# Optimization experiments

Hardware: AMD Instinct MI355X
Metric: run time of the kernel (lower is better)

Reference implementation:

```python
import jax, jax.numpy as jnp
import numpy as np

B, T, E, H = 256, 200, 512, 8
NEG = -(2.0 ** 32) + 1.0  # padding value used by the TF implementation


def _pos_table(T, E):
    # sin/cos positional encoding exactly as in PositionEncoding.build
    pos = np.arange(T)[:, None].astype(np.float64)
    i = np.arange(E)[None, :]
    angle = pos / np.power(10000.0, 2.0 * (i // 2) / E)
    pe = np.where(i % 2 == 0, np.sin(angle), np.cos(angle))
    return jnp.asarray(pe, dtype=jnp.float32)


def setup_inputs() -> dict:
    key = jax.random.key(0)
    ks = jax.random.split(key, 9)
    tn = lambda k, shape, std: (jax.random.truncated_normal(k, -2.0, 2.0, shape, jnp.float32) * std)
    glorot = lambda k, shape: jax.random.uniform(k, shape, jnp.float32,
                                                 -np.sqrt(6.0 / (shape[0] + shape[1])),
                                                 np.sqrt(6.0 / (shape[0] + shape[1])))
    return {
        "queries": jax.random.normal(ks[0], (B, T, E), jnp.float32),
        "keys": jax.random.normal(ks[1], (B, T, E), jnp.float32),
        "query_len": jax.random.randint(ks[2], (B, 1), 1, T + 1),
        "key_len": jax.random.randint(ks[3], (B, 1), 1, T + 1),
        "pos_q": _pos_table(T, E),
        "pos_k": _pos_table(T, E),
        "W_Q": tn(ks[4], (E, E), 0.05),
        "W_K": tn(ks[5], (E, E), 0.05),
        "W_V": tn(ks[6], (E, E), 0.05),
        "fw1": glorot(ks[7], (E, 4 * E)),
        "fw2": glorot(ks[8], (4 * E, E)),
    }


def reference(queries, keys, query_len, key_len, pos_q, pos_k, W_Q, W_K, W_V, fw1, fw2):
    Bq, Tq, Eq = queries.shape
    Dh = Eq // H
    dt = queries.dtype
    neg = jnp.asarray(NEG, dt)

    # positional encoding: scaled table added to inputs
    scale = jnp.asarray(Eq, dt) ** 0.5
    q_in = queries + pos_q * scale          # (B,T,E)
    k_in = keys + pos_k * scale

    # sequence masks from lengths (B,1) -> (B,T)
    ar = jnp.arange(Tq)[None, :]
    q_mask = (ar < query_len).astype(dt)
    k_mask = (ar < key_len).astype(dt)

    # projections, split into heads
    Q = (q_in @ W_Q).reshape(Bq, Tq, H, Dh)
    K_ = (k_in @ W_K).reshape(Bq, Tq, H, Dh)
    V = (k_in @ W_V).reshape(Bq, Tq, H, Dh)

    # scaled dot-product attention  (B,H,Tq,Tk)
    scores = jnp.einsum('bqhd,bkhd->bhqk', Q, K_) / jnp.asarray(Dh, dt) ** 0.5
    scores = jnp.where(k_mask[:, None, None, :] > 0, scores, neg)
    # blinding: mask the diagonal (query attends to itself)
    eye = jnp.eye(Tq, dtype=bool)
    scores = jnp.where(eye[None, None], neg, scores)
    scores = scores - jnp.max(scores, axis=-1, keepdims=True)
    attn = jax.nn.softmax(scores, axis=-1)
    attn = attn * q_mask[:, None, :, None]

    out = jnp.einsum('bhqk,bkhd->bqhd', attn, V).reshape(Bq, Tq, Eq)

    # residual (use_res=True), no layer norm (use_layer_norm=False)
    out = out + q_in

    # pointwise feed-forward + residual
    ff = jax.nn.relu(out @ fw1) @ fw2
    out = out + ff

    # output_type == 'mean'
    return jnp.mean(out, axis=1, keepdims=True)  # (B,1,E)
```

## Files before the change

### kernel.cpp

```cpp
#include <hip/hip_runtime.h>

#define B_   256
#define T_   200
#define E_   512
#define H_   8
#define Dh_  64
#define F_   2048
#define M_   (B_ * T_)
#define MH_  (M_ / 2)
#define SCALE 22.62741699796952f
#define NEGV  -4294967296.0f

typedef __attribute__((ext_vector_type(8))) short bf16x8;
typedef __attribute__((ext_vector_type(4))) float f32x4;

__device__ __forceinline__ float bf2f(unsigned short u) {
    union { unsigned u32; float f; } v; v.u32 = ((unsigned)u) << 16; return v.f;
}
__device__ __forceinline__ unsigned short f2bf(float f) {
    union { float f32; unsigned u; } v; v.f32 = f;
    unsigned r = v.u + 0x7FFFu + ((v.u >> 16) & 1u);
    return (unsigned short)(r >> 16);
}
__device__ __forceinline__ unsigned pack_hilo(float f) {
    unsigned short hi = f2bf(f);
    unsigned short lo = f2bf(f - bf2f(hi));
    return (unsigned)hi | ((unsigned)lo << 16);
}
__device__ __forceinline__ void load_lds16(const unsigned short* g, unsigned short* l) {
    __builtin_amdgcn_global_load_lds(
        (const __attribute__((address_space(1))) unsigned int*)g,
        (__attribute__((address_space(3))) unsigned int*)l, 16, 0, 0);
}

__global__ __launch_bounds__(256) void k_prep(
    float* __restrict__ q, float* __restrict__ k,
    const float* __restrict__ pos_q, const float* __restrict__ pos_k)
{
    const int z = blockIdx.y;
    float* X = z ? k : q;
    const float* Ps = z ? pos_k : pos_q;
    size_t idx = ((size_t)blockIdx.x * 256 + threadIdx.x) * 4;
    int row = (int)(idx >> 9);
    int col = (int)(idx & 511);
    int t = row % T_;
    float4 v = *(const float4*)&X[idx];
    float4 p = *(const float4*)&Ps[(size_t)t * E_ + col];
    uint4 o;
    o.x = pack_hilo(v.x + p.x * SCALE);
    o.y = pack_hilo(v.y + p.y * SCALE);
    o.z = pack_hilo(v.z + p.z * SCALE);
    o.w = pack_hilo(v.w + p.w * SCALE);
    *(uint4*)&X[idx] = o;
}

__global__ __launch_bounds__(256) void k_trw(
    const float* __restrict__ in, unsigned short* __restrict__ oh,
    unsigned short* __restrict__ ol)
{
    const int k0 = blockIdx.x * 64, n0 = blockIdx.y * 64;
    const int tid = threadIdx.x;
    __shared__ unsigned short th[64][65], tl[64][65];
#pragma unroll
    for (int i = 0; i < 16; i++) {
        int e = i * 256 + tid;
        int r = e >> 6, c = e & 63;
        float f = in[(size_t)(k0 + r) * 512 + n0 + c];
        unsigned short h = f2bf(f);
        th[r][c] = h;
        tl[r][c] = f2bf(f - bf2f(h));
    }
    __syncthreads();
#pragma unroll
    for (int i = 0; i < 16; i++) {
        int e = i * 256 + tid;
        int r = e >> 6, c = e & 63;
        oh[(size_t)(n0 + r) * 512 + k0 + c] = th[c][r];
        ol[(size_t)(n0 + r) * 512 + k0 + c] = tl[c][r];
    }
}

template<int NPROD, bool SPLIT>
__global__ __launch_bounds__(256) void k_projx(
    const unsigned int* __restrict__ Apk,
    const unsigned short* __restrict__ Bh,
    const unsigned short* __restrict__ Bl,
    unsigned short* __restrict__ Chi,
    unsigned short* __restrict__ Clo)
{
    const int K = 512, N = 512;
    __shared__ alignas(16) unsigned short AsH[128 * 32];
    __shared__ alignas(16) unsigned short AsL[128 * 32];
    __shared__ alignas(16) unsigned short BsH[128 * 32];
    __shared__ alignas(16) unsigned short BsL[(NPROD >= 3) ? 128 * 32 : 8];

    const int tid = threadIdx.x;
    const int w = tid >> 6, lane = tid & 63;
    const int m0 = blockIdx.x * 128, n0 = blockIdx.y * 128;
    const int mr = lane & 15, q = lane >> 4;

    f32x4 acc[4][4];
#pragma unroll
    for (int i = 0; i < 4; i++)
#pragma unroll
        for (int j = 0; j < 4; j++) acc[i][j] = (f32x4){0.f, 0.f, 0.f, 0.f};

    const int c0  = w * 64 + lane;
    const int c1  = 256 + w * 64 + lane;
    const int bm0 = c0 >> 2, bq0 = (c0 & 3) ^ ((bm0 >> 1) & 3);
    const int bm1 = c1 >> 2, bq1 = (c1 & 3) ^ ((bm1 >> 1) & 3);
    const unsigned short* gB0h = Bh + (size_t)(n0 + bm0) * K + bq0 * 8;
    const unsigned short* gB1h = Bh + (size_t)(n0 + bm1) * K + bq1 * 8;
    const unsigned short* gB0l = (NPROD >= 3) ? Bl + (size_t)(n0 + bm0) * K + bq0 * 8 : nullptr;
    const unsigned short* gB1l = (NPROD >= 3) ? Bl + (size_t)(n0 + bm1) * K + bq1 * 8 : nullptr;
    unsigned short* lB0h = BsH + (size_t)(w * 64) * 8;
    unsigned short* lB1h = BsH + (size_t)(256 + w * 64) * 8;
    unsigned short* lB0l = BsL + (size_t)(w * 64) * 8;
    unsigned short* lB1l = BsL + (size_t)(256 + w * 64) * 8;

    int caf[4], cbf[4];
#pragma unroll
    for (int t4 = 0; t4 < 4; t4++) {
        int ma = (w & 1) * 64 + t4 * 16 + mr;
        caf[t4] = ma * 4 + (q ^ ((ma >> 1) & 3));
        int nb = (w >> 1) * 64 + t4 * 16 + mr;
        cbf[t4] = nb * 4 + (q ^ ((nb >> 1) & 3));
    }

    for (int k0 = 0; k0 < K; k0 += 32) {
#pragma unroll
        for (int i = 0; i < 4; i++) {
            int cc = i * 256 + tid;
            int am = cc >> 3, aq = cc & 7;
            uint4 v = *(const uint4*)&Apk[(size_t)(m0 + am) * K + k0 + aq * 4];
            ushort4 h, l;
            h.x = (unsigned short)(v.x & 0xffff); l.x = (unsigned short)(v.x >> 16);
            h.y = (unsigned short)(v.y & 0xffff); l.y = (unsigned short)(v.y >> 16);
            h.z = (unsigned short)(v.z & 0xffff); l.z = (unsigned short)(v.z >> 16);
            h.w = (unsigned short)(v.w & 0xffff); l.w = (unsigned short)(v.w >> 16);
            int cp  = am * 4 + ((aq >> 1) ^ ((am >> 1) & 3));
            int off = cp * 8 + (aq & 1) * 4;
            *(ushort4*)&AsH[off] = h;
            *(ushort4*)&AsL[off] = l;
        }
        load_lds16(gB0h + k0, lB0h);
        load_lds16(gB1h + k0, lB1h);
        if (NPROD >= 3) {
            load_lds16(gB0l + k0, lB0l);
            load_lds16(gB1l + k0, lB1l);
        }
        __syncthreads();

        bf16x8 afh[4], afl[4], bgh[4], bgl[4];
#pragma unroll
        for (int t4 = 0; t4 < 4; t4++) {
            afh[t4] = *(const bf16x8*)&AsH[caf[t4] * 8];
            if (NPROD >= 2) afl[t4] = *(const bf16x8*)&AsL[caf[t4] * 8];
            bgh[t4] = *(const bf16x8*)&BsH[cbf[t4] * 8];
            if (NPROD >= 3) bgl[t4] = *(const bf16x8*)&BsL[cbf[t4] * 8];
        }
#pragma unroll
        for (int i = 0; i < 4; i++)
#pragma unroll
            for (int j = 0; j < 4; j++) {
                acc[i][j] = __builtin_amdgcn_mfma_f32_16x16x32_bf16(
                    afh[i], bgh[j], acc[i][j], 0, 0, 0);
                if (NPROD >= 3)
                    acc[i][j] = __builtin_amdgcn_mfma_f32_16x16x32_bf16(
                        afh[i], bgl[j], acc[i][j], 0, 0, 0);
                if (NPROD >= 2)
                    acc[i][j] = __builtin_amdgcn_mfma_f32_16x16x32_bf16(
                        afl[i], bgh[j], acc[i][j], 0, 0, 0);
            }
        __syncthreads();
    }

#pragma unroll
    for (int i = 0; i < 4; i++) {
        int row = m0 + (w & 1) * 64 + i * 16 + q * 4;
#pragma unroll
        for (int j = 0; j < 4; j++) {
            int col = n0 + (w >> 1) * 64 + j * 16 + mr;
#pragma unroll
            for (int r = 0; r < 4; r++) {
                float v = acc[i][j][r];
                unsigned short hi = f2bf(v);
                Chi[(size_t)(row + r) * N + col] = hi;
                if (SPLIT)
                    Clo[(size_t)(row + r) * N + col] = f2bf(v - bf2f(hi));
            }
        }
    }
}

__global__ __launch_bounds__(512, 4) void k_attn_flash(
    const unsigned short* __restrict__ Qhi, const unsigned short* __restrict__ Qlo,
    const unsigned short* __restrict__ Khi, const unsigned short* __restrict__ Klo,
    const int* __restrict__ qlen, const int* __restrict__ klen,
    const unsigned int* __restrict__ Apk,
    unsigned short* VX)
{
    const int bh = blockIdx.x;
    const int b = bh >> 3, h = bh & 7;
    const int tid = threadIdx.x;
    const int w = tid >> 6, l = tid & 63;
    const int mr = l & 15, q4 = l >> 4;

    __shared__ alignas(16) unsigned short Kh_s[2][64 * 72];
    __shared__ alignas(16) unsigned short Kl_s[2][64 * 72];
    __shared__ alignas(16) unsigned short Vt_s[2][64 * 72];
    __shared__ alignas(16) unsigned short P_s[8][16 * 72];

    const int kl = klen[b], ql = qlen[b];
    const int cmax = (kl > 1) ? ((kl + 63) >> 6) : 4;

    auto stage = [&](int cs, int sb) {
#pragma unroll
        for (int ii = 0; ii < 2; ii++) {
            const int idx = ii * 512 + tid;
            const int jn = idx >> 4, dq = idx & 15;
            const int n = cs * 64 + jn;
            if (n < T_) {
                const size_t g = (size_t)(b * T_ + n) * E_ + h * 64 + dq * 4;
                *(uint2*)&Kh_s[sb][jn * 72 + dq * 4] = *(const uint2*)&Khi[g];
                *(uint2*)&Kl_s[sb][jn * 72 + dq * 4] = *(const uint2*)&Klo[g];
                ushort4 v = *(const ushort4*)&VX[g];
                Vt_s[sb][(dq * 4 + 0) * 72 + jn] = v.x;
                Vt_s[sb][(dq * 4 + 1) * 72 + jn] = v.y;
                Vt_s[sb][(dq * 4 + 2) * 72 + jn] = v.z;
                Vt_s[sb][(dq * 4 + 3) * 72 + jn] = v.w;
            } else {
                Vt_s[sb][(dq * 4 + 0) * 72 + jn] = 0;
                Vt_s[sb][(dq * 4 + 1) * 72 + jn] = 0;
                Vt_s[sb][(dq * 4 + 2) * 72 + jn] = 0;
                Vt_s[sb][(dq * 4 + 3) * 72 + jn] = 0;
            }
        }
    };

    bf16x8 qh0[2], qh1[2];
#pragma unroll
    for (int j = 0; j < 2; j++) {
        const int qt = w + 8 * j;
        if (qt < 13 && qt * 16 < ql) {
            const size_t qoff = (size_t)(b * T_ + qt * 16 + mr) * E_ + h * 64 + q4 * 8;
            qh0[j] = *(const bf16x8*)&Qhi[qoff];
            qh1[j] = *(const bf16x8*)&Qhi[qoff + 32];
        }
    }

    f32x4 O[2][4];
    float m_r[2][4], l_r[2][4];
#pragma unroll
    for (int j = 0; j < 2; j++) {
#pragma unroll
        for (int nt = 0; nt < 4; nt++) O[j][nt] = (f32x4){0.f, 0.f, 0.f, 0.f};
#pragma unroll
        for (int r = 0; r < 4; r++) { m_r[j][r] = -INFINITY; l_r[j][r] = 0.f; }
    }

    stage(0, 0);
    __syncthreads();

    for (int c = 0; c < cmax; c++) {
        const int pb = c & 1;
        if (c + 1 < cmax) stage(c + 1, pb ^ 1);

#pragma unroll
        for (int j = 0; j < 2; j++) {
            const int qt = w + 8 * j;
            if (qt < 13 && qt * 16 < ql) {
                const int q0 = qt * 16;
                const size_t qoff = (size_t)(b * T_ + q0 + mr) * E_ + h * 64 + q4 * 8;
                bf16x8 qe0 = *(const bf16x8*)&Qlo[qoff];
                bf16x8 qe1 = *(const bf16x8*)&Qlo[qoff + 32];

                f32x4 a[4];
#pragma unroll
                for (int kt = 0; kt < 4; kt++) a[kt] = (f32x4){0.f, 0.f, 0.f, 0.f};
                __builtin_amdgcn_s_setprio(1);
#pragma unroll
                for (int kt = 0; kt < 4; kt++) {
                    if (c * 64 + kt * 16 < 208) {
                        const int rbase = (kt * 16 + mr) * 72 + q4 * 8;
                        bf16x8 kh0 = *(const bf16x8*)&Kh_s[pb][rbase];
                        bf16x8 kh1 = *(const bf16x8*)&Kh_s[pb][rbase + 32];
                        bf16x8 ke0 = *(const bf16x8*)&Kl_s[pb][rbase];
                        bf16x8 ke1 = *(const bf16x8*)&Kl_s[pb][rbase + 32];
                        a[kt] = __builtin_amdgcn_mfma_f32_16x16x32_bf16(qh0[j], kh0, a[kt], 0, 0, 0);
                        a[kt] = __builtin_amdgcn_mfma_f32_16x16x32_bf16(qh1[j], kh1, a[kt], 0, 0, 0);
                        a[kt] = __builtin_amdgcn_mfma_f32_16x16x32_bf16(qh0[j], ke0, a[kt], 0, 0, 0);
                        a[kt] = __builtin_amdgcn_mfma_f32_16x16x32_bf16(qh1[j], ke1, a[kt], 0, 0, 0);
                        a[kt] = __builtin_amdgcn_mfma_f32_16x16x32_bf16(qe0, kh0, a[kt], 0, 0, 0);
                        a[kt] = __builtin_amdgcn_mfma_f32_16x16x32_bf16(qe1, kh1, a[kt], 0, 0, 0);
                    }
                }
                __builtin_amdgcn_s_setprio(0);

                float mc[4] = {-INFINITY, -INFINITY, -INFINITY, -INFINITY};
#pragma unroll
                for (int kt = 0; kt < 4; kt++) {
                    int col = c * 64 + kt * 16 + mr;
#pragma unroll
                    for (int r = 0; r < 4; r++) {
                        int row = q0 + q4 * 4 + r;
                        float v = a[kt][r] * 0.125f;
                        if (col >= kl)  v = NEGV;
                        if (col == row) v = NEGV;
                        if (col >= T_)  v = -INFINITY;
                        a[kt][r] = v;
                        mc[r] = fmaxf(mc[r], v);
                    }
                }
#pragma unroll
                for (int r = 0; r < 4; r++)
#pragma unroll
                    for (int off = 1; off < 16; off <<= 1)
                        mc[r] = fmaxf(mc[r], __shfl_xor(mc[r], off));
                float mn[4], alpha[4], ps[4];
#pragma unroll
                for (int r = 0; r < 4; r++) {
                    mn[r] = fmaxf(m_r[j][r], mc[r]);
                    alpha[r] = __expf(m_r[j][r] - mn[r]);
                    ps[r] = 0.f;
                }
#pragma unroll
                for (int kt = 0; kt < 4; kt++)
#pragma unroll
                    for (int r = 0; r < 4; r++) {
                        float p = __expf(a[kt][r] - mn[r]);
                        a[kt][r] = p;
                        ps[r] += p;
                    }
#pragma unroll
                for (int r = 0; r < 4; r++)
#pragma unroll
                    for (int off = 1; off < 16; off <<= 1)
                        ps[r] += __shfl_xor(ps[r], off);
#pragma unroll
                for (int r = 0; r < 4; r++) {
                    l_r[j][r] = l_r[j][r] * alpha[r] + ps[r];
                    m_r[j][r] = mn[r];
                }
#pragma unroll
                for (int nt = 0; nt < 4; nt++)
#pragma unroll
                    for (int r = 0; r < 4; r++) O[j][nt][r] *= alpha[r];
#pragma unroll
                for (int kt = 0; kt < 4; kt++)
#pragma unroll
                    for (int r = 0; r < 4; r++)
                        P_s[w][(q4 * 4 + r) * 72 + kt * 16 + mr] = f2bf(a[kt][r]);
                __builtin_amdgcn_s_setprio(1);
#pragma unroll
                for (int k2 = 0; k2 < 2; k2++) {
                    bf16x8 pf = *(const bf16x8*)&P_s[w][mr * 72 + k2 * 32 + q4 * 8];
#pragma unroll
                    for (int nt = 0; nt < 4; nt++) {
                        bf16x8 vf = *(const bf16x8*)&Vt_s[pb][(nt * 16 + mr) * 72 + k2 * 32 + q4 * 8];
                        O[j][nt] = __builtin_amdgcn_mfma_f32_16x16x32_bf16(pf, vf, O[j][nt], 0, 0, 0);
                    }
                }
                __builtin_amdgcn_s_setprio(0);
            }
        }
        __syncthreads();
    }

#pragma unroll
    for (int j = 0; j < 2; j++) {
        const int qt = w + 8 * j;
        if (qt < 13) {
#pragma unroll
            for (int r = 0; r < 4; r++) {
                int row = qt * 16 + q4 * 4 + r;
                if (row < T_) {
                    float inv = (row < ql) ? (1.f / l_r[j][r]) : 0.f;
#pragma unroll
                    for (int nt = 0; nt < 4; nt++) {
                        int d = nt * 16 + mr;
                        size_t gi = (size_t)(b * T_ + row) * E_ + h * 64 + d;
                        unsigned u = Apk[gi];
                        float res = bf2f((unsigned short)(u & 0xffff)) +
                                    bf2f((unsigned short)(u >> 16));
                        VX[gi] = f2bf(O[j][nt][r] * inv + res);
                    }
                }
            }
        }
    }
}

__global__ __launch_bounds__(256) void k_tr(
    const float* __restrict__ in, unsigned short* __restrict__ out, int K, int N)
{
    const int k0 = blockIdx.x * 64, n0 = blockIdx.y * 64;
    const int tid = threadIdx.x;
    __shared__ unsigned short t[64][65];
#pragma unroll
    for (int i = 0; i < 16; i++) {
        int e = i * 256 + tid;
        int r = e >> 6, c = e & 63;
        t[r][c] = f2bf(in[(size_t)(k0 + r) * N + n0 + c]);
    }
    __syncthreads();
#pragma unroll
    for (int i = 0; i < 16; i++) {
        int e = i * 256 + tid;
        int r = e >> 6, c = e & 63;
        out[(size_t)(n0 + r) * K + k0 + c] = t[c][r];
    }
}

template<int K, int N, bool RELU, bool RES>
__global__ __launch_bounds__(256) void k_gemm_bt(
    const unsigned short* __restrict__ A,
    const unsigned short* __restrict__ Bt,
    unsigned short* __restrict__ C,
    const unsigned short* __restrict__ Res)
{
    __shared__ alignas(16) unsigned short As[128 * 32];
    __shared__ alignas(16) unsigned short Bs[128 * 32];

    const int tid  = threadIdx.x;
    const int w    = tid >> 6, lane = tid & 63;
    const int m0   = blockIdx.x * 128, n0 = blockIdx.y * 128;
    const int mr   = lane & 15, q = lane >> 4;

    f32x4 acc[4][4];
#pragma unroll
    for (int i = 0; i < 4; i++)
#pragma unroll
        for (int j = 0; j < 4; j++) acc[i][j] = (f32x4){0.f, 0.f, 0.f, 0.f};

    const int c0  = w * 64 + lane;
    const int c1  = 256 + w * 64 + lane;
    const int am0 = c0 >> 2, aq0 = (c0 & 3) ^ ((am0 >> 1) & 3);
    const int am1 = c1 >> 2, aq1 = (c1 & 3) ^ ((am1 >> 1) & 3);
    const unsigned short* gA0 = A  + (size_t)(m0 + am0) * K + aq0 * 8;
    const unsigned short* gA1 = A  + (size_t)(m0 + am1) * K + aq1 * 8;
    const unsigned short* gB0 = Bt + (size_t)(n0 + am0) * K + aq0 * 8;
    const unsigned short* gB1 = Bt + (size_t)(n0 + am1) * K + aq1 * 8;
    unsigned short* lA0 = As + (size_t)(w * 64) * 8;
    unsigned short* lA1 = As + (size_t)(256 + w * 64) * 8;
    unsigned short* lB0 = Bs + (size_t)(w * 64) * 8;
    unsigned short* lB1 = Bs + (size_t)(256 + w * 64) * 8;

    int caf[4], cbf[4];
#pragma unroll
    for (int t4 = 0; t4 < 4; t4++) {
        int ma = (w & 1) * 64 + t4 * 16 + mr;
        caf[t4] = ma * 4 + (q ^ ((ma >> 1) & 3));
        int nb = (w >> 1) * 64 + t4 * 16 + mr;
        cbf[t4] = nb * 4 + (q ^ ((nb >> 1) & 3));
    }

    for (int k0 = 0; k0 < K; k0 += 32) {
        load_lds16(gA0 + k0, lA0);
        load_lds16(gA1 + k0, lA1);
        load_lds16(gB0 + k0, lB0);
        load_lds16(gB1 + k0, lB1);
        __syncthreads();

        bf16x8 af[4], bg[4];
#pragma unroll
        for (int t4 = 0; t4 < 4; t4++) {
            af[t4] = *(const bf16x8*)&As[caf[t4] * 8];
            bg[t4] = *(const bf16x8*)&Bs[cbf[t4] * 8];
        }
#pragma unroll
        for (int i = 0; i < 4; i++)
#pragma unroll
            for (int j = 0; j < 4; j++)
                acc[i][j] = __builtin_amdgcn_mfma_f32_16x16x32_bf16(
                    af[i], bg[j], acc[i][j], 0, 0, 0);
        __syncthreads();
    }

#pragma unroll
    for (int i = 0; i < 4; i++) {
        int row = m0 + (w & 1) * 64 + i * 16 + q * 4;
#pragma unroll
        for (int j = 0; j < 4; j++) {
            int col = n0 + (w >> 1) * 64 + j * 16 + mr;
#pragma unroll
            for (int r = 0; r < 4; r++) {
                float v = acc[i][j][r];
                if (RELU) v = fmaxf(v, 0.f);
                if (RES)  v += bf2f(Res[(size_t)(row + r) * N + col]);
                C[(size_t)(row + r) * N + col] = f2bf(v);
            }
        }
    }
}

__global__ __launch_bounds__(256) void k_mean(
    const unsigned short* __restrict__ out2, float* __restrict__ out)
{
    const int b = blockIdx.x;
    const int w = threadIdx.x >> 6, lane = threadIdx.x & 63;
    float s[8] = {0.f, 0.f, 0.f, 0.f, 0.f, 0.f, 0.f, 0.f};
    for (int t = w; t < T_; t += 4) {
        bf16x8 v = *(const bf16x8*)&out2[(size_t)(b * T_ + t) * E_ + lane * 8];
#pragma unroll
        for (int j = 0; j < 8; j++) s[j] += bf2f((unsigned short)v[j]);
    }
    __shared__ float red[4][512];
#pragma unroll
    for (int j = 0; j < 8; j++) red[w][lane * 8 + j] = s[j];
    __syncthreads();
#pragma unroll
    for (int e = threadIdx.x; e < 512; e += 256)
        out[(size_t)b * E_ + e] =
            (red[0][e] + red[1][e] + red[2][e] + red[3][e]) * (1.0f / 200.0f);
}

extern "C" void kernel_launch(void* const* d_in, const int* in_sizes, int n_in,
                              void* d_out, int out_size, void* d_ws, size_t ws_size,
                              hipStream_t stream)
{
    float* qmut = (float*)d_in[0];
    float* kmut = (float*)d_in[1];
    const int*   qlen  = (const int*)d_in[2];
    const int*   klen  = (const int*)d_in[3];
    const float* pos_q = (const float*)d_in[4];
    const float* pos_k = (const float*)d_in[5];
    const float* W_Q   = (const float*)d_in[6];
    const float* W_K   = (const float*)d_in[7];
    const float* W_V   = (const float*)d_in[8];
    const float* fw1   = (const float*)d_in[9];
    const float* fw2   = (const float*)d_in[10];
    float* out = (float*)d_out;

    char* base = (char*)d_ws;
    unsigned short* Qhi = (unsigned short*)base;
    unsigned short* Qlo = (unsigned short*)(base +  52428800);
    unsigned short* Khi = (unsigned short*)(base + 104857600);
    unsigned short* Klo = (unsigned short*)(base + 157286400);
    unsigned short* VX  = (unsigned short*)(base + 209715200);

    unsigned short* wQh = VX;
    unsigned short* wQl = VX + 262144;
    unsigned short* wKh = VX + 524288;
    unsigned short* wKl = VX + 786432;
    unsigned short* wVh = (unsigned short*)W_Q;
    unsigned short* wVl = (unsigned short*)W_Q + 262144;

    unsigned short* Hbuf   = (unsigned short*)base;
    unsigned short* out2bf = (unsigned short*)(base + 104857600);
    unsigned short* fw1t   = (unsigned short*)(base + 157286400);
    unsigned short* fw2t   = (unsigned short*)(base + 159383552);

    const unsigned int* Aq = (const unsigned int*)qmut;
    const unsigned int* Ak = (const unsigned int*)kmut;

    k_prep<<<dim3(M_ * E_ / 1024, 2), 256, 0, stream>>>(qmut, kmut, pos_q, pos_k);
    k_trw<<<dim3(8, 8), 256, 0, stream>>>(W_Q, wQh, wQl);
    k_trw<<<dim3(8, 8), 256, 0, stream>>>(W_K, wKh, wKl);
    k_projx<3, true><<<dim3(M_ / 128, 4), 256, 0, stream>>>(Aq, wQh, wQl, Qhi, Qlo);
    k_projx<3, true><<<dim3(M_ / 128, 4), 256, 0, stream>>>(Ak, wKh, wKl, Khi, Klo);
    k_trw<<<dim3(8, 8), 256, 0, stream>>>(W_V, wVh, wVl);
    k_projx<2, false><<<dim3(M_ / 128, 4), 256, 0, stream>>>(Ak, wVh, nullptr, VX, nullptr);

    k_attn_flash<<<B_ * H_, 512, 0, stream>>>(
        Qhi, Qlo, Khi, Klo, qlen, klen, Aq, VX);

    k_tr<<<dim3(E_ / 64, F_ / 64), 256, 0, stream>>>(fw1, fw1t, E_, F_);
    k_tr<<<dim3(F_ / 64, E_ / 64), 256, 0, stream>>>(fw2, fw2t, F_, E_);

    for (int c = 0; c < 2; c++) {
        const unsigned short* Xc = VX + (size_t)c * MH_ * E_;
        unsigned short* Oc = out2bf + (size_t)c * MH_ * E_;
        k_gemm_bt<E_, F_, true, false><<<dim3(MH_ / 128, F_ / 128), 256, 0, stream>>>(
            Xc, fw1t, Hbuf, nullptr);
        k_gemm_bt<F_, E_, false, true><<<dim3(MH_ / 128, E_ / 128), 256, 0, stream>>>(
            Hbuf, fw2t, Oc, Xc);
    }
    k_mean<<<B_, 256, 0, stream>>>(out2bf, out);
}
```

Before: 1.018 ms.

## Reduce ReLU activations over time before the second FFN matmul, skipping per-token fw2 GEMM

Because the final output is a mean over time and fw2 is linear, the ReLU(X·fw1) activations are summed per batch inside the first GEMM's epilogue with atomics. A small (256×2048)·(2048×512) GEMM then replaces the full per-token second FFN GEMM, and the residual mean is computed separately. The projection kernel also loads packed hi/lo A operands straight into LDS with async global-to-LDS copies and unpacks them at fragment-read time. This removes the large H buffer write/read and most of the fw2 FLOPs, at the cost of float atomics, which make the summation order nondeterministic.

Result: faster. 923.6 us (-9.2%).

```diff
diff --git a/kernel.cpp b/kernel.cpp
--- a/kernel.cpp
+++ b/kernel.cpp
@@ -7,7 +7,6 @@
 #define Dh_  64
 #define F_   2048
 #define M_   (B_ * T_)
-#define MH_  (M_ / 2)
 #define SCALE 22.62741699796952f
 #define NEGV  -4294967296.0f
 
@@ -27,7 +26,7 @@
     unsigned short lo = f2bf(f - bf2f(hi));
     return (unsigned)hi | ((unsigned)lo << 16);
 }
-__device__ __forceinline__ void load_lds16(const unsigned short* g, unsigned short* l) {
+__device__ __forceinline__ void load_lds16(const void* g, void* l) {
     __builtin_amdgcn_global_load_lds(
         (const __attribute__((address_space(1))) unsigned int*)g,
         (__attribute__((address_space(3))) unsigned int*)l, 16, 0, 0);
@@ -80,7 +79,7 @@
     }
 }
 
-template<int NPROD, bool SPLIT>
+template<int K, int NPROD, bool SPLIT, bool FOUT>
 __global__ __launch_bounds__(256) void k_projx(
     const unsigned int* __restrict__ Apk,
     const unsigned short* __restrict__ Bh,
@@ -88,16 +87,15 @@
     unsigned short* __restrict__ Chi,
     unsigned short* __restrict__ Clo)
 {
-    const int K = 512, N = 512;
-    __shared__ alignas(16) unsigned short AsH[128 * 32];
-    __shared__ alignas(16) unsigned short AsL[128 * 32];
+    const int N = 512;
+    __shared__ alignas(16) unsigned int   Asp[128 * 32];
     __shared__ alignas(16) unsigned short BsH[128 * 32];
     __shared__ alignas(16) unsigned short BsL[(NPROD >= 3) ? 128 * 32 : 8];
 
     const int tid = threadIdx.x;
     const int w = tid >> 6, lane = tid & 63;
     const int m0 = blockIdx.x * 128, n0 = blockIdx.y * 128;
-    const int mr = lane & 15, q = lane >> 4;
+    const int mr = lane & 15, q4 = lane >> 4;
 
     f32x4 acc[4][4];
 #pragma unroll
@@ -105,8 +103,17 @@
 #pragma unroll
         for (int j = 0; j < 4; j++) acc[i][j] = (f32x4){0.f, 0.f, 0.f, 0.f};
 
+    const unsigned int* gA[4];
+    unsigned int* lA[4];
+#pragma unroll
+    for (int it = 0; it < 4; it++) {
+        int c = it * 256 + tid;
+        int row = c >> 3, cc = c & 7;
+        gA[it] = Apk + (size_t)(m0 + row) * K + ((cc ^ (row & 7)) * 4);
+        lA[it] = Asp + (size_t)(it * 256 + w * 64) * 4;
+    }
     const int c0  = w * 64 + lane;
-    const int c1  = 256 + w * 64 + lane;
+    const int c1  = 256 + c0;
     const int bm0 = c0 >> 2, bq0 = (c0 & 3) ^ ((bm0 >> 1) & 3);
     const int bm1 = c1 >> 2, bq1 = (c1 & 3) ^ ((bm1 >> 1) & 3);
     const unsigned short* gB0h = Bh + (size_t)(n0 + bm0) * K + bq0 * 8;
@@ -118,31 +125,17 @@
     unsigned short* lB0l = BsL + (size_t)(w * 64) * 8;
     unsigned short* lB1l = BsL + (size_t)(256 + w * 64) * 8;
 
-    int caf[4], cbf[4];
+    int cbf[4];
 #pragma unroll
     for (int t4 = 0; t4 < 4; t4++) {
-        int ma = (w & 1) * 64 + t4 * 16 + mr;
-        caf[t4] = ma * 4 + (q ^ ((ma >> 1) & 3));
         int nb = (w >> 1) * 64 + t4 * 16 + mr;
-        cbf[t4] = nb * 4 + (q ^ ((nb >> 1) & 3));
-    }
+        cbf[t4] = nb * 4 + (q4 ^ ((nb >> 1) & 3));
+    }
+    const int ra_base = (w & 1) * 64;
 
     for (int k0 = 0; k0 < K; k0 += 32) {
 #pragma unroll
-        for (int i = 0; i < 4; i++) {
-            int cc = i * 256 + tid;
-            int am = cc >> 3, aq = cc & 7;
-            uint4 v = *(const uint4*)&Apk[(size_t)(m0 + am) * K + k0 + aq * 4];
-            ushort4 h, l;
-            h.x = (unsigned short)(v.x & 0xffff); l.x = (unsigned short)(v.x >> 16);
-            h.y = (unsigned short)(v.y & 0xffff); l.y = (unsigned short)(v.y >> 16);
-            h.z = (unsigned short)(v.z & 0xffff); l.z = (unsigned short)(v.z >> 16);
-            h.w = (unsigned short)(v.w & 0xffff); l.w = (unsigned short)(v.w >> 16);
-            int cp  = am * 4 + ((aq >> 1) ^ ((am >> 1) & 3));
-            int off = cp * 8 + (aq & 1) * 4;
-            *(ushort4*)&AsH[off] = h;
-            *(ushort4*)&AsL[off] = l;
-        }
+        for (int it = 0; it < 4; it++) load_lds16(gA[it] + k0, lA[it]);
         load_lds16(gB0h + k0, lB0h);
         load_lds16(gB1h + k0, lB1h);
         if (NPROD >= 3) {
@@ -154,8 +147,21 @@
         bf16x8 afh[4], afl[4], bgh[4], bgl[4];
 #pragma unroll
         for (int t4 = 0; t4 < 4; t4++) {
-            afh[t4] = *(const bf16x8*)&AsH[caf[t4] * 8];
-            if (NPROD >= 2) afl[t4] = *(const bf16x8*)&AsL[caf[t4] * 8];
+            const int ra = ra_base + t4 * 16 + mr;
+            const int r7 = ra & 7;
+            uint4 u0 = *(const uint4*)&Asp[(size_t)(ra * 8 + ((q4 * 2) ^ r7)) * 4];
+            uint4 u1 = *(const uint4*)&Asp[(size_t)(ra * 8 + ((q4 * 2 + 1) ^ r7)) * 4];
+            union { unsigned u[4]; bf16x8 v; } Hh, Ll;
+            Hh.u[0] = (u0.x & 0xffffu) | (u0.y << 16);
+            Hh.u[1] = (u0.z & 0xffffu) | (u0.w << 16);
+            Hh.u[2] = (u1.x & 0xffffu) | (u1.y << 16);
+            Hh.u[3] = (u1.z & 0xffffu) | (u1.w << 16);
+            afh[t4] = Hh.v;
+            Ll.u[0] = (u0.x >> 16) | (u0.y & 0xffff0000u);
+            Ll.u[1] = (u0.z >> 16) | (u0.w & 0xffff0000u);
+            Ll.u[2] = (u1.x >> 16) | (u1.y & 0xffff0000u);
+            Ll.u[3] = (u1.z >> 16) | (u1.w & 0xffff0000u);
+            afl[t4] = Ll.v;
             bgh[t4] = *(const bf16x8*)&BsH[cbf[t4] * 8];
             if (NPROD >= 3) bgl[t4] = *(const bf16x8*)&BsL[cbf[t4] * 8];
         }
@@ -168,26 +174,29 @@
                 if (NPROD >= 3)
                     acc[i][j] = __builtin_amdgcn_mfma_f32_16x16x32_bf16(
                         afh[i], bgl[j], acc[i][j], 0, 0, 0);
-                if (NPROD >= 2)
-                    acc[i][j] = __builtin_amdgcn_mfma_f32_16x16x32_bf16(
-                        afl[i], bgh[j], acc[i][j], 0, 0, 0);
+                acc[i][j] = __builtin_amdgcn_mfma_f32_16x16x32_bf16(
+                    afl[i], bgh[j], acc[i][j], 0, 0, 0);
             }
         __syncthreads();
     }
 
 #pragma unroll
     for (int i = 0; i < 4; i++) {
-        int row = m0 + (w & 1) * 64 + i * 16 + q * 4;
+        int row = m0 + (w & 1) * 64 + i * 16 + (lane >> 4) * 4;
 #pragma unroll
         for (int j = 0; j < 4; j++) {
             int col = n0 + (w >> 1) * 64 + j * 16 + mr;
 #pragma unroll
             for (int r = 0; r < 4; r++) {
                 float v = acc[i][j][r];
-                unsigned short hi = f2bf(v);
-                Chi[(size_t)(row + r) * N + col] = hi;
-                if (SPLIT)
-                    Clo[(size_t)(row + r) * N + col] = f2bf(v - bf2f(hi));
+                if (FOUT) {
+                    ((float*)Chi)[(size_t)(row + r) * N + col] = v;
+                } else {
+                    unsigned short hi = f2bf(v);
+                    Chi[(size_t)(row + r) * N + col] = hi;
+                    if (SPLIT)
+                        Clo[(size_t)(row + r) * N + col] = f2bf(v - bf2f(hi));
+                }
             }
         }
     }
@@ -412,15 +421,15 @@
     }
 }
 
-template<int K, int N, bool RELU, bool RES>
-__global__ __launch_bounds__(256) void k_gemm_bt(
+__global__ __launch_bounds__(256) void k_gemm_relusum(
     const unsigned short* __restrict__ A,
     const unsigned short* __restrict__ Bt,
-    unsigned short* __restrict__ C,
-    const unsigned short* __restrict__ Res)
-{
+    float* __restrict__ Hsum)
+{
+    const int K = E_, N = F_;
     __shared__ alignas(16) unsigned short As[128 * 32];
     __shared__ alignas(16) unsigned short Bs[128 * 32];
+    __shared__ float colsum[2][128];
 
     const int tid  = threadIdx.x;
     const int w    = tid >> 6, lane = tid & 63;
@@ -477,31 +486,61 @@
         __syncthreads();
     }
 
-#pragma unroll
-    for (int i = 0; i < 4; i++) {
-        int row = m0 + (w & 1) * 64 + i * 16 + q * 4;
-#pragma unroll
-        for (int j = 0; j < 4; j++) {
-            int col = n0 + (w >> 1) * 64 + j * 16 + mr;
+    ((float*)colsum)[tid] = 0.f;
+    __syncthreads();
+    const int b0 = m0 / 200;
+    const int bsplit = (b0 + 1) * 200;
+#pragma unroll
+    for (int j = 0; j < 4; j++) {
+        const int colr = (w >> 1) * 64 + j * 16 + mr;
+        float s0 = 0.f, s1 = 0.f;
+#pragma unroll
+        for (int i = 0; i < 4; i++) {
+            const int rowb = m0 + (w & 1) * 64 + i * 16 + q * 4;
 #pragma unroll
             for (int r = 0; r < 4; r++) {
-                float v = acc[i][j][r];
-                if (RELU) v = fmaxf(v, 0.f);
-                if (RES)  v += bf2f(Res[(size_t)(row + r) * N + col]);
-                C[(size_t)(row + r) * N + col] = f2bf(v);
+                float v = fmaxf(acc[i][j][r], 0.f);
+                if (rowb + r >= bsplit) s1 += v; else s0 += v;
             }
         }
-    }
-}
-
-__global__ __launch_bounds__(256) void k_mean(
-    const unsigned short* __restrict__ out2, float* __restrict__ out)
+        atomicAdd(&colsum[0][colr], s0);
+        atomicAdd(&colsum[1][colr], s1);
+    }
+    __syncthreads();
+    if (tid < 128) {
+        atomicAdd(&Hsum[(size_t)b0 * N + n0 + tid], colsum[0][tid]);
+        if (bsplit < m0 + 128)
+            atomicAdd(&Hsum[(size_t)(b0 + 1) * N + n0 + tid], colsum[1][tid]);
+    }
+}
+
+__global__ __launch_bounds__(256) void k_zero(float* __restrict__ p)
+{
+    ((float4*)p)[(size_t)blockIdx.x * 256 + threadIdx.x] = (float4){0.f, 0.f, 0.f, 0.f};
+}
+
+__global__ __launch_bounds__(256) void k_hm(
+    const float* __restrict__ Hsum, unsigned int* __restrict__ Hmpk)
+{
+    size_t idx = ((size_t)blockIdx.x * 256 + threadIdx.x) * 4;
+    float4 v = *(const float4*)&Hsum[idx];
+    uint4 o;
+    o.x = pack_hilo(v.x * (1.0f / 200.0f));
+    o.y = pack_hilo(v.y * (1.0f / 200.0f));
+    o.z = pack_hilo(v.z * (1.0f / 200.0f));
+    o.w = pack_hilo(v.w * (1.0f / 200.0f));
+    *(uint4*)&Hmpk[idx] = o;
+}
+
+__global__ __launch_bounds__(256) void k_final(
+    const unsigned short* __restrict__ X, const float* __restrict__ ffm,
+    float* __restrict__ out)
 {
     const int b = blockIdx.x;
     const int w = threadIdx.x >> 6, lane = threadIdx.x & 63;
     float s[8] = {0.f, 0.f, 0.f, 0.f, 0.f, 0.f, 0.f, 0.f};
     for (int t = w; t < T_; t += 4) {
-        bf16x8 v = *(const bf16x8*)&out2[(size_t)(b * T_ + t) * E_ + lane * 8];
+        bf16x8 v = *(const bf16x8*)&X[(size_t)(b * T_ + t) * E_ + lane * 8];
 #pragma unroll
         for (int j = 0; j < 8; j++) s[j] += bf2f((unsigned short)v[j]);
     }
@@ -509,10 +548,10 @@
 #pragma unroll
     for (int j = 0; j < 8; j++) red[w][lane * 8 + j] = s[j];
     __syncthreads();
-#pragma unroll
     for (int e = threadIdx.x; e < 512; e += 256)
         out[(size_t)b * E_ + e] =
-            (red[0][e] + red[1][e] + red[2][e] + red[3][e]) * (1.0f / 200.0f);
+            (red[0][e] + red[1][e] + red[2][e] + red[3][e]) * (1.0f / 200.0f) +
+            ffm[(size_t)b * E_ + e];
 }
 
 extern "C" void kernel_launch(void* const* d_in, const int* in_sizes, int n_in,
@@ -546,10 +585,11 @@
     unsigned short* wVh = (unsigned short*)W_Q;
     unsigned short* wVl = (unsigned short*)W_Q + 262144;
 
-    unsigned short* Hbuf   = (unsigned short*)base;
-    unsigned short* out2bf = (unsigned short*)(base + 104857600);
-    unsigned short* fw1t   = (unsigned short*)(base + 157286400);
-    unsigned short* fw2t   = (unsigned short*)(base + 159383552);
+    unsigned short* fw1t = (unsigned short*)(base + 157286400);
+    unsigned short* fw2t = (unsigned short*)(base + 159383552);
+    float*        Hsum = (float*)(base + 161480704);
+    unsigned int* Hmpk = (unsigned int*)(base + 163577856);
+    float*        ffm  = (float*)(base + 165675008);
 
     const unsigned int* Aq = (const unsigned int*)qmut;
     const unsigned int* Ak = (const unsigned int*)kmut;
@@ -557,24 +597,24 @@
     k_prep<<<dim3(M_ * E_ / 1024, 2), 256, 0, stream>>>(qmut, kmut, pos_q, pos_k);
     k_trw<<<dim3(8, 8), 256, 0, stream>>>(W_Q, wQh, wQl);
     k_trw<<<dim3(8, 8), 256, 0, stream>>>(W_K, wKh, wKl);
-    k_projx<3, true><<<dim3(M_ / 128, 4), 256, 0, stream>>>(Aq, wQh, wQl, Qhi, Qlo);
-    k_projx<3, true><<<dim3(M_ / 128, 4), 256, 0, stream>>>(Ak, wKh, wKl, Khi, Klo);
+    k_projx<512, 3, true, false><<<dim3(M_ / 128, 4), 256, 0, stream>>>(
+        Aq, wQh, wQl, Qhi, Qlo);
+    k_projx<512, 3, true, false><<<dim3(M_ / 128, 4), 256, 0, stream>>>(
+        Ak, wKh, wKl, Khi, Klo);
     k_trw<<<dim3(8, 8), 256, 0, stream>>>(W_V, wVh, wVl);
-    k_projx<2, false><<<dim3(M_ / 128, 4), 256, 0, stream>>>(Ak, wVh, nullptr, VX, nullptr);
+    k_projx<512, 2, false, false><<<dim3(M_ / 128, 4), 256, 0, stream>>>(
+        Ak, wVh, nullptr, VX, nullptr);
 
     k_attn_flash<<<B_ * H_, 512, 0, stream>>>(
         Qhi, Qlo, Khi, Klo, qlen, klen, Aq, VX);
 
     k_tr<<<dim3(E_ / 64, F_ / 64), 256, 0, stream>>>(fw1, fw1t, E_, F_);
     k_tr<<<dim3(F_ / 64, E_ / 64), 256, 0, stream>>>(fw2, fw2t, F_, E_);
-
-    for (int c = 0; c < 2; c++) {
-        const unsigned short* Xc = VX + (size_t)c * MH_ * E_;
-        unsigned short* Oc = out2bf + (size_t)c * MH_ * E_;
-        k_gemm_bt<E_, F_, true, false><<<dim3(MH_ / 128, F_ / 128), 256, 0, stream>>>(
-            Xc, fw1t, Hbuf, nullptr);
-        k_gemm_bt<F_, E_, false, true><<<dim3(MH_ / 128, E_ / 128), 256, 0, stream>>>(
-            Hbuf, fw2t, Oc, Xc);
-    }
-    k_mean<<<B_, 256, 0, stream>>>(out2bf, out);
-}
+    k_zero<<<512, 256, 0, stream>>>(Hsum);
+
+    k_gemm_relusum<<<dim3(M_ / 128, F_ / 128), 256, 0, stream>>>(VX, fw1t, Hsum);
+    k_hm<<<512, 256, 0, stream>>>(Hsum, Hmpk);
+    k_projx<2048, 2, false, true><<<dim3(2, 4), 256, 0, stream>>>(
+        Hmpk, fw2t, nullptr, (unsigned short*)ffm, nullptr);
+    k_final<<<B_, 256, 0, stream>>>(VX, ffm, out);
+}
```
